# Performance work log

Hardware: AMD Instinct MI355X
Metric: run time of the kernel (lower is better)

Reference implementation:

```python
import jax, jax.numpy as jnp
import numpy as np

B, S, D = 4, 4096, 64

def setup_inputs() -> dict:
    key = jax.random.key(0)
    kq, kk, kv = jax.random.split(key, 3)
    return {
        "q": jax.random.normal(kq, (B, S, D), dtype=jnp.float32),
        "k": jax.random.normal(kk, (B, S, D), dtype=jnp.float32),
        "v": jax.random.normal(kv, (B, S, D), dtype=jnp.float32),
    }

def reference(q, k, v):
    # scores: [B, Sq, Sk]; NOTE: scale is k.shape[-1] (not sqrt), per the source.
    scores = jnp.einsum("bqd,bkd->bqk", q, k) / k.shape[-1]
    # softmax over dim=1 == the QUERY axis (non-standard), then matmul V.
    probs = jax.nn.softmax(scores, axis=1)            # [B, Sq, Sk]
    attn = jnp.einsum("bqk,bkd->bqd", probs, v)       # [B, Sq, D]
    attn_w = jax.nn.softmax(attn, axis=1)             # softmax over Sq again
    return (attn, attn_w)
```

## Files before the change

kernel.cpp:

```cpp
#include <hip/hip_runtime.h>
#include <hip/hip_bf16.h>
#include <math.h>

#define BB 4
#define SS 4096
#define DD 64
#define KSPLIT 4
#define QSPLIT 8

typedef __attribute__((ext_vector_type(8))) short short8;
typedef __attribute__((ext_vector_type(4))) float f32x4;
typedef __attribute__((ext_vector_type(2))) unsigned int u32x2;
typedef unsigned int u32;
typedef unsigned short ushort_t;

#define MFMA16(a,b,c) __builtin_amdgcn_mfma_f32_16x16x32_bf16((a),(b),(c),0,0,0)
#define C2SC 0.022542110700140054f

static __device__ __forceinline__ unsigned short f2bf(float f) {
  union { float f; u32 u; } x; x.f = f;
  u32 r = (x.u + 0x7FFFu + ((x.u >> 16) & 1u)) >> 16;
  return (unsigned short)r;
}

static __device__ __forceinline__ u32 pk2(float a, float b) {
  __hip_bfloat16 lo = __float2bfloat16(a);
  __hip_bfloat16 hi = __float2bfloat16(b);
  unsigned short ls, hs;
  __builtin_memcpy(&ls, &lo, 2); __builtin_memcpy(&hs, &hi, 2);
  return (u32)ls | ((u32)hs << 16);
}

static __device__ __forceinline__ void gload16(const void* g, void* l) {
  __builtin_amdgcn_global_load_lds((const __attribute__((address_space(1))) u32*)g,
                                   (__attribute__((address_space(3))) u32*)l, 16, 0, 0);
}

__global__ __launch_bounds__(256) void p0_convert(
    const float* __restrict__ q, const float* __restrict__ k,
    ushort_t* __restrict__ QB, ushort_t* __restrict__ KB,
    float* __restrict__ out0, float* __restrict__ z2)
{
  const size_t i = (size_t)blockIdx.x * 256 + threadIdx.x;
  float4 a = ((const float4*)q)[i];
  float4 c = ((const float4*)k)[i];
  ((ushort4*)QB)[i] = make_ushort4(f2bf(a.x), f2bf(a.y), f2bf(a.z), f2bf(a.w));
  ((ushort4*)KB)[i] = make_ushort4(f2bf(c.x), f2bf(c.y), f2bf(c.z), f2bf(c.w));
  ((float4*)out0)[i] = make_float4(0.f, 0.f, 0.f, 0.f);
  if (blockIdx.x == 0) z2[threadIdx.x] = 0.f;
}

__global__ __launch_bounds__(256) void pa_colsum(
    const ushort_t* __restrict__ QB, const ushort_t* __restrict__ KB,
    float* __restrict__ Zp)
{
  const int kb0 = blockIdx.x * 64;
  const int qch = blockIdx.y;
  const int b   = blockIdx.z;
  const int t = threadIdx.x, w = t >> 6, lane = t & 63;
  const int g = lane >> 4, r15 = lane & 15;
  const int r8 = lane >> 3, c8 = lane & 7;
  const int QCH = SS / QSPLIT;
  const int NT = QCH / 64;

  __shared__ alignas(16) char qbuf[2][64*128];

  short8 ak[2];
  {
    const ushort_t* p = KB + ((size_t)b * SS + kb0 + 16*w + r15) * DD;
#pragma unroll
    for (int dh = 0; dh < 2; ++dh) ak[dh] = *(const short8*)(p + 32*dh + 8*g);
  }

  {
    const int q0 = qch * QCH;
#pragma unroll
    for (int j = 0; j < 2; ++j) {
      const int rl = 16*w + 8*j + r8;
      const char* gsrc = (const char*)(QB + ((size_t)b*SS + q0 + rl)*DD) + 16*(c8 ^ r8);
      gload16(gsrc, qbuf[0] + (16*w + 8*j)*128);
    }
  }
  asm volatile("s_waitcnt vmcnt(0)" ::: "memory");
  __syncthreads();

  float z0=0.f, z1=0.f, z2v=0.f, z3=0.f;
  int cur = 0;
  for (int tt = 0; tt < NT; ++tt) {
    if (tt < NT-1) {
      const int q0 = qch*QCH + (tt+1)*64;
#pragma unroll
      for (int j = 0; j < 2; ++j) {
        const int rl = 16*w + 8*j + r8;
        const char* gsrc = (const char*)(QB + ((size_t)b*SS + q0 + rl)*DD) + 16*(c8 ^ r8);
        gload16(gsrc, qbuf[cur^1] + (16*w + 8*j)*128);
      }
    }
    const char* qb = qbuf[cur];
#pragma unroll
    for (int qt = 0; qt < 4; ++qt) {
      f32x4 acc = {0.f,0.f,0.f,0.f};
      const int qrow = 16*qt + r15;
      const char* base = qb + qrow*128;
#pragma unroll
      for (int dh = 0; dh < 2; ++dh) {
        short8 bq = *(const short8*)(base + 16*((4*dh + g) ^ (qrow & 7)));
        acc = MFMA16(ak[dh], bq, acc);
      }
      z0 += exp2f(acc[0]*C2SC); z1 += exp2f(acc[1]*C2SC);
      z2v += exp2f(acc[2]*C2SC); z3 += exp2f(acc[3]*C2SC);
    }
    asm volatile("s_waitcnt vmcnt(0)" ::: "memory");
    __syncthreads();
    cur ^= 1;
  }
#pragma unroll
  for (int m = 1; m < 16; m <<= 1) {
    z0 += __shfl_xor(z0, m); z1 += __shfl_xor(z1, m);
    z2v += __shfl_xor(z2v, m); z3 += __shfl_xor(z3, m);
  }
  if (r15 == 0) {
    float* dst = Zp + ((size_t)qch*BB + b)*SS + kb0 + 16*w + 4*g;
    dst[0]=z0; dst[1]=z1; dst[2]=z2v; dst[3]=z3;
  }
}

__global__ __launch_bounds__(256) void p2_vt(
    const float* __restrict__ v, const float* __restrict__ Zp,
    ushort_t* __restrict__ VT)
{
  const int k0 = blockIdx.x * 64;
  const int b  = blockIdx.y;
  const int t = threadIdx.x;
  __shared__ float vs[64][65];
  __shared__ float izs[64];
  {
    const int row = t >> 2, cq = (t & 3) * 16;
    const float* src = v + ((size_t)b*SS + k0 + row)*DD + cq;
#pragma unroll
    for (int i = 0; i < 4; ++i) {
      float4 x = ((const float4*)src)[i];
      vs[row][cq + 4*i + 0] = x.x; vs[row][cq + 4*i + 1] = x.y;
      vs[row][cq + 4*i + 2] = x.z; vs[row][cq + 4*i + 3] = x.w;
    }
  }
  if (t < 64) {
    float z = 0.f;
#pragma unroll
    for (int c = 0; c < QSPLIT; ++c)
      z += Zp[((size_t)c*BB + b)*SS + k0 + t];
    izs[t] = 1.0f / z;
  }
  __syncthreads();
  const int d = t >> 2, ks = (t & 3) * 16;
  u32* dst = (u32*)VT + (((size_t)b*DD + d)*SS + k0 + ks)/2;
#pragma unroll
  for (int i = 0; i < 8; ++i) {
    float a0 = vs[ks + 2*i    ][d] * izs[ks + 2*i    ];
    float a1 = vs[ks + 2*i + 1][d] * izs[ks + 2*i + 1];
    dst[i] = (u32)f2bf(a0) | ((u32)f2bf(a1) << 16);
  }
}

__global__ __launch_bounds__(256) void pb_attn(
    const ushort_t* __restrict__ QB, const ushort_t* __restrict__ KB,
    const ushort_t* __restrict__ VT, float* __restrict__ out0)
{
  const int q0 = blockIdx.x * 64;
  const int kbase = blockIdx.y * (SS / KSPLIT);
  const int b  = blockIdx.z;
  const int t = threadIdx.x, w = t >> 6, lane = t & 63;
  const int g = lane >> 4, r15 = lane & 15;
  const int r8 = lane >> 3, c8 = lane & 7;
  const int NT = SS / KSPLIT / 64;

  __shared__ alignas(16) char kbuf[2][64*128];
  __shared__ alignas(16) char vbuf[2][64*128];
  __shared__ alignas(16) char plds[4][16*128];

  short8 aq[2];
  {
    const ushort_t* p = QB + ((size_t)b*SS + q0 + 16*w + r15) * DD;
#pragma unroll
    for (int dh = 0; dh < 2; ++dh) aq[dh] = *(const short8*)(p + 32*dh + 8*g);
  }

#pragma unroll
  for (int j = 0; j < 2; ++j) {
    const int rl = 16*w + 8*j + r8;
    const char* gk = (const char*)(KB + ((size_t)b*SS + kbase + rl)*DD) + 16*(c8 ^ r8);
    gload16(gk, kbuf[0] + (16*w+8*j)*128);
    const char* gv = (const char*)(VT + ((size_t)b*DD + rl)*SS + kbase) + 16*(c8 ^ r8);
    gload16(gv, vbuf[0] + (16*w+8*j)*128);
  }
  asm volatile("s_waitcnt vmcnt(0)" ::: "memory");
  __syncthreads();

  f32x4 accA[4];
#pragma unroll
  for (int dt = 0; dt < 4; ++dt) accA[dt] = (f32x4){0.f,0.f,0.f,0.f};

  char* pw = plds[w];
  int cur = 0;
  for (int kt = 0; kt < NT; ++kt) {
    if (kt < NT-1) {
      const int kc = kbase + (kt+1)*64;
#pragma unroll
      for (int j = 0; j < 2; ++j) {
        const int rl = 16*w + 8*j + r8;
        const char* gk = (const char*)(KB + ((size_t)b*SS + kc + rl)*DD) + 16*(c8 ^ r8);
        gload16(gk, kbuf[cur^1] + (16*w+8*j)*128);
        const char* gv = (const char*)(VT + ((size_t)b*DD + rl)*SS + kc) + 16*(c8 ^ r8);
        gload16(gv, vbuf[cur^1] + (16*w+8*j)*128);
      }
    }
    const char* kb = kbuf[cur];
    const char* vb = vbuf[cur];

#pragma unroll
    for (int ct = 0; ct < 4; ++ct) {
      f32x4 accs = {0.f,0.f,0.f,0.f};
      const int krow = 16*ct + r15;
      const char* base = kb + krow*128;
#pragma unroll
      for (int dh = 0; dh < 2; ++dh) {
        short8 ak = *(const short8*)(base + 16*((4*dh+g) ^ (krow&7)));
        accs = MFMA16(ak, aq[dh], accs);
      }
      u32 p01 = pk2(exp2f(accs[0]*C2SC), exp2f(accs[1]*C2SC));
      u32 p23 = pk2(exp2f(accs[2]*C2SC), exp2f(accs[3]*C2SC));
      const u32 off = ((u32)(32*ct + 8*g)) ^ (((u32)(r15 & 7)) << 4);
      *(u32x2*)(pw + r15*128 + off) = (u32x2){p01, p23};
    }

#pragma unroll
    for (int ks = 0; ks < 2; ++ks) {
      const u32 poff = ((u32)(64*ks + 16*g)) ^ (((u32)(r15 & 7)) << 4);
      short8 ap = *(const short8*)(pw + r15*128 + poff);
#pragma unroll
      for (int dt = 0; dt < 4; ++dt) {
        const int drow = 16*dt + r15;
        short8 bv = *(const short8*)(vb + drow*128 + 16*((4*ks+g) ^ (drow&7)));
        accA[dt] = MFMA16(ap, bv, accA[dt]);
      }
    }
    asm volatile("s_waitcnt vmcnt(0)" ::: "memory");
    __syncthreads();
    cur ^= 1;
  }

#pragma unroll
  for (int dt = 0; dt < 4; ++dt)
#pragma unroll
    for (int rr = 0; rr < 4; ++rr)
      atomicAdd(&out0[((size_t)b*SS + q0 + 16*w + 4*g + rr)*DD + 16*dt + r15],
                accA[dt][rr]);
}

__global__ __launch_bounds__(256) void k4f(
    const float* __restrict__ attn, float* __restrict__ z2)
{
  const int b = blockIdx.x;
  const int q0 = blockIdx.y * 64;
  const int t = threadIdx.x;
  const int d = t & 63, rg = t >> 6;
  float ze = 0.f;
#pragma unroll
  for (int i = 0; i < 16; ++i) {
    float a = attn[((size_t)b*SS + q0 + 4*i + rg)*DD + d];
    ze += __expf(a);
  }
  __shared__ float red[4][64];
  red[rg][d] = ze;
  __syncthreads();
  if (t < 64)
    atomicAdd(&z2[b*DD + t], red[0][t] + red[1][t] + red[2][t] + red[3][t]);
}

__global__ __launch_bounds__(256) void k6w(
    const float* __restrict__ attn, const float* __restrict__ z2,
    float* __restrict__ out1)
{
  const size_t i = (size_t)blockIdx.x * 256 + threadIdx.x;
  const int b = (int)(i >> 18);
  const int d = (int)(i & 63);
  out1[i] = __expf(attn[i]) / z2[b*DD + d];
}

extern "C" void kernel_launch(void* const* d_in, const int* in_sizes, int n_in,
                              void* d_out, int out_size, void* d_ws, size_t ws_size,
                              hipStream_t stream) {
  const float* q = (const float*)d_in[0];
  const float* k = (const float*)d_in[1];
  const float* v = (const float*)d_in[2];
  float* out0 = (float*)d_out;
  float* out1 = out0 + (size_t)BB * SS * DD;

  ushort_t* QB = (ushort_t*)out1;
  ushort_t* KB = QB + (size_t)BB * SS * DD;

  float* ws = (float*)d_ws;
  ushort_t* VT = (ushort_t*)ws;
  float* Zp = (float*)(VT + (size_t)BB * DD * SS);
  float* z2 = Zp + (size_t)QSPLIT * BB * SS;

  hipLaunchKernelGGL(p0_convert, dim3(BB*SS*DD/4/256), dim3(256), 0, stream, q, k, QB, KB, out0, z2);
  hipLaunchKernelGGL(pa_colsum, dim3(SS/64, QSPLIT, BB), dim3(256), 0, stream, QB, KB, Zp);
  hipLaunchKernelGGL(p2_vt, dim3(SS/64, BB), dim3(256), 0, stream, v, Zp, VT);
  hipLaunchKernelGGL(pb_attn, dim3(SS/64, KSPLIT, BB), dim3(256), 0, stream, QB, KB, VT, out0);
  hipLaunchKernelGGL(k4f, dim3(BB, SS/64), dim3(256), 0, stream, out0, z2);
  hipLaunchKernelGGL(k6w, dim3(BB*SS*DD/256), dim3(256), 0, stream, out0, z2, out1);
}
```

Before: 83.23 us.

## Restructure attention kernel with register-resident P tiles and wider column-sum tiles

pb_attn is rewritten so each wave handles all 64 queries against its own 16-key slice of a 128-key tile. The P fragments stay in registers instead of round-tripping through LDS, double-buffering is dropped, and the four waves reduce their partial outputs through LDS before a single wave issues the atomics. pa_colsum now gives each wave two 16-key slices so each Q fragment loaded from LDS is reused twice. Also changed: the bf16 packing now uses a manual round, and k4f gets more blocks with fewer rows each. The cost is more accumulator registers, an unpipelined load-wait in every pb_attn iteration, and a serial cross-wave reduction at the end.

```diff
diff --git a/kernel.cpp b/kernel.cpp
--- a/kernel.cpp
+++ b/kernel.cpp
@@ -17,6 +17,8 @@
 #define MFMA16(a,b,c) __builtin_amdgcn_mfma_f32_16x16x32_bf16((a),(b),(c),0,0,0)
 #define C2SC 0.022542110700140054f
 
+union Pk8 { short8 s8; u32 u[4]; u32x2 h[2]; };
+
 static __device__ __forceinline__ unsigned short f2bf(float f) {
   union { float f; u32 u; } x; x.f = f;
   u32 r = (x.u + 0x7FFFu + ((x.u >> 16) & 1u)) >> 16;
@@ -24,11 +26,7 @@
 }
 
 static __device__ __forceinline__ u32 pk2(float a, float b) {
-  __hip_bfloat16 lo = __float2bfloat16(a);
-  __hip_bfloat16 hi = __float2bfloat16(b);
-  unsigned short ls, hs;
-  __builtin_memcpy(&ls, &lo, 2); __builtin_memcpy(&hs, &hi, 2);
-  return (u32)ls | ((u32)hs << 16);
+  return (u32)f2bf(a) | ((u32)f2bf(b) << 16);
 }
 
 static __device__ __forceinline__ void gload16(const void* g, void* l) {
@@ -50,11 +48,11 @@
   if (blockIdx.x == 0) z2[threadIdx.x] = 0.f;
 }
 
-__global__ __launch_bounds__(256) void pa_colsum(
+__global__ __launch_bounds__(256, 4) void pa_colsum(
     const ushort_t* __restrict__ QB, const ushort_t* __restrict__ KB,
     float* __restrict__ Zp)
 {
-  const int kb0 = blockIdx.x * 64;
+  const int kb0 = blockIdx.x * 128;
   const int qch = blockIdx.y;
   const int b   = blockIdx.z;
   const int t = threadIdx.x, w = t >> 6, lane = t & 63;
@@ -65,12 +63,12 @@
 
   __shared__ alignas(16) char qbuf[2][64*128];
 
-  short8 ak[2];
-  {
-    const ushort_t* p = KB + ((size_t)b * SS + kb0 + 16*w + r15) * DD;
-#pragma unroll
-    for (int dh = 0; dh < 2; ++dh) ak[dh] = *(const short8*)(p + 32*dh + 8*g);
-  }
+  short8 ak[2][2];
+#pragma unroll
+  for (int s = 0; s < 2; ++s)
+#pragma unroll
+    for (int dh = 0; dh < 2; ++dh)
+      ak[s][dh] = *(const short8*)(KB + ((size_t)b*SS + kb0 + 32*w + 16*s + r15)*DD + 32*dh + 8*g);
 
   {
     const int q0 = qch * QCH;
@@ -84,7 +82,10 @@
   asm volatile("s_waitcnt vmcnt(0)" ::: "memory");
   __syncthreads();
 
-  float z0=0.f, z1=0.f, z2v=0.f, z3=0.f;
+  float z[8];
+#pragma unroll
+  for (int i = 0; i < 8; ++i) z[i] = 0.f;
+
   int cur = 0;
   for (int tt = 0; tt < NT; ++tt) {
     if (tt < NT-1) {
@@ -99,29 +100,33 @@
     const char* qb = qbuf[cur];
 #pragma unroll
     for (int qt = 0; qt < 4; ++qt) {
-      f32x4 acc = {0.f,0.f,0.f,0.f};
       const int qrow = 16*qt + r15;
       const char* base = qb + qrow*128;
-#pragma unroll
-      for (int dh = 0; dh < 2; ++dh) {
-        short8 bq = *(const short8*)(base + 16*((4*dh + g) ^ (qrow & 7)));
-        acc = MFMA16(ak[dh], bq, acc);
+      short8 bq0 = *(const short8*)(base + 16*((g    ) ^ (qrow & 7)));
+      short8 bq1 = *(const short8*)(base + 16*((4 + g) ^ (qrow & 7)));
+#pragma unroll
+      for (int s = 0; s < 2; ++s) {
+        f32x4 acc = {0.f,0.f,0.f,0.f};
+        acc = MFMA16(ak[s][0], bq0, acc);
+        acc = MFMA16(ak[s][1], bq1, acc);
+        z[4*s+0] += exp2f(acc[0]*C2SC); z[4*s+1] += exp2f(acc[1]*C2SC);
+        z[4*s+2] += exp2f(acc[2]*C2SC); z[4*s+3] += exp2f(acc[3]*C2SC);
       }
-      z0 += exp2f(acc[0]*C2SC); z1 += exp2f(acc[1]*C2SC);
-      z2v += exp2f(acc[2]*C2SC); z3 += exp2f(acc[3]*C2SC);
     }
     asm volatile("s_waitcnt vmcnt(0)" ::: "memory");
     __syncthreads();
     cur ^= 1;
   }
 #pragma unroll
-  for (int m = 1; m < 16; m <<= 1) {
-    z0 += __shfl_xor(z0, m); z1 += __shfl_xor(z1, m);
-    z2v += __shfl_xor(z2v, m); z3 += __shfl_xor(z3, m);
-  }
+  for (int m = 1; m < 16; m <<= 1)
+#pragma unroll
+    for (int i = 0; i < 8; ++i) z[i] += __shfl_xor(z[i], m);
   if (r15 == 0) {
-    float* dst = Zp + ((size_t)qch*BB + b)*SS + kb0 + 16*w + 4*g;
-    dst[0]=z0; dst[1]=z1; dst[2]=z2v; dst[3]=z3;
+#pragma unroll
+    for (int s = 0; s < 2; ++s)
+#pragma unroll
+      for (int r = 0; r < 4; ++r)
+        Zp[((size_t)qch*BB + b)*SS + kb0 + 32*w + 16*s + 4*g + r] = z[4*s+r];
   }
 }
 
@@ -162,7 +167,7 @@
   }
 }
 
-__global__ __launch_bounds__(256) void pb_attn(
+__global__ __launch_bounds__(256, 3) void pb_attn(
     const ushort_t* __restrict__ QB, const ushort_t* __restrict__ KB,
     const ushort_t* __restrict__ VT, float* __restrict__ out0)
 {
@@ -171,102 +176,132 @@
   const int b  = blockIdx.z;
   const int t = threadIdx.x, w = t >> 6, lane = t & 63;
   const int g = lane >> 4, r15 = lane & 15;
-  const int r8 = lane >> 3, c8 = lane & 7;
-  const int NT = SS / KSPLIT / 64;
-
-  __shared__ alignas(16) char kbuf[2][64*128];
-  __shared__ alignas(16) char vbuf[2][64*128];
-  __shared__ alignas(16) char plds[4][16*128];
-
-  short8 aq[2];
-  {
-    const ushort_t* p = QB + ((size_t)b*SS + q0 + 16*w + r15) * DD;
-#pragma unroll
-    for (int dh = 0; dh < 2; ++dh) aq[dh] = *(const short8*)(p + 32*dh + 8*g);
-  }
-
-#pragma unroll
-  for (int j = 0; j < 2; ++j) {
-    const int rl = 16*w + 8*j + r8;
-    const char* gk = (const char*)(KB + ((size_t)b*SS + kbase + rl)*DD) + 16*(c8 ^ r8);
-    gload16(gk, kbuf[0] + (16*w+8*j)*128);
-    const char* gv = (const char*)(VT + ((size_t)b*DD + rl)*SS + kbase) + 16*(c8 ^ r8);
-    gload16(gv, vbuf[0] + (16*w+8*j)*128);
-  }
-  asm volatile("s_waitcnt vmcnt(0)" ::: "memory");
-  __syncthreads();
-
-  f32x4 accA[4];
-#pragma unroll
-  for (int dt = 0; dt < 4; ++dt) accA[dt] = (f32x4){0.f,0.f,0.f,0.f};
-
-  char* pw = plds[w];
-  int cur = 0;
+  const int NT = SS / KSPLIT / 128;
+
+  __shared__ alignas(16) char kbuf[128*128];
+  __shared__ alignas(16) char vbuf[64*256];
+
+  short8 aq[4][2];
+#pragma unroll
+  for (int qt = 0; qt < 4; ++qt)
+#pragma unroll
+    for (int dh = 0; dh < 2; ++dh)
+      aq[qt][dh] = *(const short8*)(QB + ((size_t)b*SS + q0 + 16*qt + r15)*DD + 32*dh + 8*g);
+
+  f32x4 acc[4][4];
+#pragma unroll
+  for (int qt = 0; qt < 4; ++qt)
+#pragma unroll
+    for (int dt = 0; dt < 4; ++dt) acc[qt][dt] = (f32x4){0.f,0.f,0.f,0.f};
+
   for (int kt = 0; kt < NT; ++kt) {
-    if (kt < NT-1) {
-      const int kc = kbase + (kt+1)*64;
-#pragma unroll
-      for (int j = 0; j < 2; ++j) {
-        const int rl = 16*w + 8*j + r8;
-        const char* gk = (const char*)(KB + ((size_t)b*SS + kc + rl)*DD) + 16*(c8 ^ r8);
-        gload16(gk, kbuf[cur^1] + (16*w+8*j)*128);
-        const char* gv = (const char*)(VT + ((size_t)b*DD + rl)*SS + kc) + 16*(c8 ^ r8);
-        gload16(gv, vbuf[cur^1] + (16*w+8*j)*128);
-      }
-    }
-    const char* kb = kbuf[cur];
-    const char* vb = vbuf[cur];
-
-#pragma unroll
-    for (int ct = 0; ct < 4; ++ct) {
-      f32x4 accs = {0.f,0.f,0.f,0.f};
-      const int krow = 16*ct + r15;
-      const char* base = kb + krow*128;
-#pragma unroll
-      for (int dh = 0; dh < 2; ++dh) {
-        short8 ak = *(const short8*)(base + 16*((4*dh+g) ^ (krow&7)));
-        accs = MFMA16(ak, aq[dh], accs);
-      }
-      u32 p01 = pk2(exp2f(accs[0]*C2SC), exp2f(accs[1]*C2SC));
-      u32 p23 = pk2(exp2f(accs[2]*C2SC), exp2f(accs[3]*C2SC));
-      const u32 off = ((u32)(32*ct + 8*g)) ^ (((u32)(r15 & 7)) << 4);
-      *(u32x2*)(pw + r15*128 + off) = (u32x2){p01, p23};
-    }
-
-#pragma unroll
-    for (int ks = 0; ks < 2; ++ks) {
-      const u32 poff = ((u32)(64*ks + 16*g)) ^ (((u32)(r15 & 7)) << 4);
-      short8 ap = *(const short8*)(pw + r15*128 + poff);
-#pragma unroll
-      for (int dt = 0; dt < 4; ++dt) {
-        const int drow = 16*dt + r15;
-        short8 bv = *(const short8*)(vb + drow*128 + 16*((4*ks+g) ^ (drow&7)));
-        accA[dt] = MFMA16(ap, bv, accA[dt]);
-      }
+    const int k0 = kbase + kt*128;
+#pragma unroll
+    for (int j = 0; j < 4; ++j) {
+      const int row = 32*j + 8*w + (lane >> 3);
+      const char* gsrc = (const char*)(KB + ((size_t)b*SS + k0 + row)*DD) + 16*((lane & 7) ^ (row & 7));
+      gload16(gsrc, kbuf + (32*j + 8*w)*128);
+    }
+#pragma unroll
+    for (int j = 0; j < 4; ++j) {
+      const int row = 16*j + 4*w + (lane >> 4);
+      const char* gsrc = (const char*)(VT + ((size_t)b*DD + row)*SS + k0) + 16*((lane & 15) ^ (row & 15));
+      gload16(gsrc, vbuf + (16*j + 4*w)*256);
     }
     asm volatile("s_waitcnt vmcnt(0)" ::: "memory");
     __syncthreads();
-    cur ^= 1;
-  }
-
-#pragma unroll
-  for (int dt = 0; dt < 4; ++dt)
-#pragma unroll
-    for (int rr = 0; rr < 4; ++rr)
-      atomicAdd(&out0[((size_t)b*SS + q0 + 16*w + 4*g + rr)*DD + 16*dt + r15],
-                accA[dt][rr]);
+
+    u32 pk[2][4][2];
+#pragma unroll
+    for (int s = 0; s < 2; ++s) {
+      const int rowA = 64*s + 16*w + r15;
+      const char* base = kbuf + rowA*128;
+      short8 ka0 = *(const short8*)(base + 16*((g    ) ^ (rowA & 7)));
+      short8 ka1 = *(const short8*)(base + 16*((4 + g) ^ (rowA & 7)));
+#pragma unroll
+      for (int qt = 0; qt < 4; ++qt) {
+        f32x4 a = {0.f,0.f,0.f,0.f};
+        a = MFMA16(ka0, aq[qt][0], a);
+        a = MFMA16(ka1, aq[qt][1], a);
+        pk[s][qt][0] = pk2(exp2f(a[0]*C2SC), exp2f(a[1]*C2SC));
+        pk[s][qt][1] = pk2(exp2f(a[2]*C2SC), exp2f(a[3]*C2SC));
+      }
+    }
+    Pk8 ap[4];
+#pragma unroll
+    for (int qt = 0; qt < 4; ++qt) {
+      ap[qt].u[0] = pk[0][qt][0]; ap[qt].u[1] = pk[0][qt][1];
+      ap[qt].u[2] = pk[1][qt][0]; ap[qt].u[3] = pk[1][qt][1];
+    }
+    const int cA = 2*w + (g >> 1);
+    const int cB = 8 + 2*w + (g >> 1);
+    const int sub8 = 8*(g & 1);
+#pragma unroll
+    for (int dt = 0; dt < 4; ++dt) {
+      const int vrow = 16*dt + r15;
+      Pk8 bv;
+      bv.h[0] = *(const u32x2*)(vbuf + vrow*256 + 16*(cA ^ r15) + sub8);
+      bv.h[1] = *(const u32x2*)(vbuf + vrow*256 + 16*(cB ^ r15) + sub8);
+#pragma unroll
+      for (int qt = 0; qt < 4; ++qt)
+        acc[qt][dt] = MFMA16(ap[qt].s8, bv.s8, acc[qt][dt]);
+    }
+    __syncthreads();
+  }
+
+  f32x4* r0 = (f32x4*)kbuf;
+  f32x4* r1 = (f32x4*)vbuf;
+  if (w == 1) {
+#pragma unroll
+    for (int qt = 0; qt < 4; ++qt)
+#pragma unroll
+      for (int dt = 0; dt < 4; ++dt) r0[(qt*4+dt)*64 + lane] = acc[qt][dt];
+  }
+  if (w == 2) {
+#pragma unroll
+    for (int qt = 0; qt < 4; ++qt)
+#pragma unroll
+      for (int dt = 0; dt < 4; ++dt) r1[(qt*4+dt)*64 + lane] = acc[qt][dt];
+  }
+  __syncthreads();
+  if (w == 0) {
+#pragma unroll
+    for (int qt = 0; qt < 4; ++qt)
+#pragma unroll
+      for (int dt = 0; dt < 4; ++dt)
+        acc[qt][dt] += r0[(qt*4+dt)*64 + lane] + r1[(qt*4+dt)*64 + lane];
+  }
+  __syncthreads();
+  if (w == 3) {
+#pragma unroll
+    for (int qt = 0; qt < 4; ++qt)
+#pragma unroll
+      for (int dt = 0; dt < 4; ++dt) r0[(qt*4+dt)*64 + lane] = acc[qt][dt];
+  }
+  __syncthreads();
+  if (w == 0) {
+#pragma unroll
+    for (int qt = 0; qt < 4; ++qt)
+#pragma unroll
+      for (int dt = 0; dt < 4; ++dt) {
+        f32x4 s = acc[qt][dt] + r0[(qt*4+dt)*64 + lane];
+#pragma unroll
+        for (int rr = 0; rr < 4; ++rr)
+          atomicAdd(&out0[((size_t)b*SS + q0 + 16*qt + 4*g + rr)*DD + 16*dt + r15], s[rr]);
+      }
+  }
 }
 
 __global__ __launch_bounds__(256) void k4f(
     const float* __restrict__ attn, float* __restrict__ z2)
 {
   const int b = blockIdx.x;
-  const int q0 = blockIdx.y * 64;
+  const int q0 = blockIdx.y * 32;
   const int t = threadIdx.x;
   const int d = t & 63, rg = t >> 6;
   float ze = 0.f;
 #pragma unroll
-  for (int i = 0; i < 16; ++i) {
+  for (int i = 0; i < 8; ++i) {
     float a = attn[((size_t)b*SS + q0 + 4*i + rg)*DD + d];
     ze += __expf(a);
   }
@@ -305,9 +340,9 @@
   float* z2 = Zp + (size_t)QSPLIT * BB * SS;
 
   hipLaunchKernelGGL(p0_convert, dim3(BB*SS*DD/4/256), dim3(256), 0, stream, q, k, QB, KB, out0, z2);
-  hipLaunchKernelGGL(pa_colsum, dim3(SS/64, QSPLIT, BB), dim3(256), 0, stream, QB, KB, Zp);
+  hipLaunchKernelGGL(pa_colsum, dim3(SS/128, QSPLIT, BB), dim3(256), 0, stream, QB, KB, Zp);
   hipLaunchKernelGGL(p2_vt, dim3(SS/64, BB), dim3(256), 0, stream, v, Zp, VT);
   hipLaunchKernelGGL(pb_attn, dim3(SS/64, KSPLIT, BB), dim3(256), 0, stream, QB, KB, VT, out0);
-  hipLaunchKernelGGL(k4f, dim3(BB, SS/64), dim3(256), 0, stream, out0, z2);
+  hipLaunchKernelGGL(k4f, dim3(BB, SS/32), dim3(256), 0, stream, out0, z2);
   hipLaunchKernelGGL(k6w, dim3(BB*SS*DD/256), dim3(256), 0, stream, out0, z2, out1);
 }
```

Result: slower. 87.79 us (+5.5%).
